# Performance work log

Measured on AMD Instinct MI355X. Metric: run time of the kernel, lower is better.

The kernel has to match this reference:

```python
import jax, jax.numpy as jnp
import numpy as np

T, H, I, E, K = 2048, 1024, 1024, 16, 4
ALPHA, LIMIT, EPS = 1.702, 7.0, 1e-5


def setup_inputs() -> dict:
    key = jax.random.key(0)
    ks = jax.random.split(key, 8)
    s = 0.02  # init scale for weights
    return {
        "x": jax.random.normal(ks[0], (T, H), jnp.float32),
        "norm_scale": jnp.ones((H,), jnp.float32),
        "gate_w": jax.random.normal(ks[1], (E, H), jnp.float32) * s,
        "gate_b": jax.random.normal(ks[2], (E,), jnp.float32) * s,
        "mlp1_w": jax.random.normal(ks[3], (E, 2 * I, H), jnp.float32) * s,
        "mlp1_b": jax.random.normal(ks[4], (E, 2 * I), jnp.float32) * s,
        "mlp2_w": jax.random.normal(ks[5], (E, H, I), jnp.float32) * s,
        "mlp2_b": jax.random.normal(ks[6], (E, H), jnp.float32) * s,
    }


def rmsnorm(x, scale):
    t = x * jax.lax.rsqrt(jnp.mean(x * x, axis=-1, keepdims=True) + EPS)
    return t * scale


def swiglu(h):
    # interleaved gating: even channels -> glu, odd channels -> linear
    glu = jnp.minimum(h[..., ::2], LIMIT)
    lin = jnp.clip(h[..., 1::2], -LIMIT, LIMIT)
    return glu * jax.nn.sigmoid(ALPHA * glu) * (lin + 1.0)


def reference(x, norm_scale, gate_w, gate_b, mlp1_w, mlp1_b, mlp2_w, mlp2_b):
    t = rmsnorm(x, norm_scale)                                   # [T,H]
    g = t @ gate_w.T + gate_b                                    # [T,E]
    vals, idx = jax.lax.top_k(g, K)                              # [T,K]
    w = jax.nn.softmax(vals, axis=-1)                            # [T,K]
    # Dense per-expert FFN (same math as per-token weight gather, computed
    # once per expert then selected -- avoids materializing [T,K,2I,H]).
    h = jnp.einsum('th,ech->tec', t, mlp1_w) + mlp1_b            # [T,E,2I]
    act = swiglu(h)                                              # [T,E,I]
    y = jnp.einsum('tei,ehi->teh', act, mlp2_w) + mlp2_b         # [T,E,H]
    y_sel = jnp.take_along_axis(y, idx[:, :, None], axis=1)      # [T,K,H]
    return x + jnp.einsum('tkh,tk->th', y_sel, w)
```

## Files before the change

### kernel.cpp

```cpp
#include <hip/hip_runtime.h>
#include <hip/hip_bf16.h>
#include <stdint.h>

typedef unsigned short u16;
typedef __attribute__((ext_vector_type(8))) short short8;
typedef __attribute__((ext_vector_type(4))) float f32x4;

#define T_TOK 2048
#define H_DIM 1024
#define E_NUM 16
#define TWO_I 2048
#define I_DIM 1024
#define ALPHA 1.702f
#define LIMIT 7.0f
#define CNT_STRIDE 64

__device__ __forceinline__ u16 f2b(float f) {
    uint32_t x = __builtin_bit_cast(uint32_t, f);
    uint32_t r = x + 0x7fffu + ((x >> 16) & 1u);
    return (u16)(r >> 16);
}
__device__ __forceinline__ short8 pack8(float4 a, float4 b) {
    short8 r;
    r[0] = (short)f2b(a.x); r[1] = (short)f2b(a.y);
    r[2] = (short)f2b(a.z); r[3] = (short)f2b(a.w);
    r[4] = (short)f2b(b.x); r[5] = (short)f2b(b.y);
    r[6] = (short)f2b(b.z); r[7] = (short)f2b(b.w);
    return r;
}

template<typename BT> struct BFrag;
template<> struct BFrag<u16> {
    short8 v;
    __device__ __forceinline__ void load(const u16* p) { v = *(const short8*)p; }
    __device__ __forceinline__ short8 get() const { return v; }
};
template<> struct BFrag<float> {
    float4 a, b;
    __device__ __forceinline__ void load(const float* p) {
        const float4* q = (const float4*)p; a = q[0]; b = q[1];
    }
    __device__ __forceinline__ short8 get() const { return pack8(a, b); }
};

__global__ __launch_bounds__(256) void cvt_kernel(
    const float* __restrict__ in, u16* __restrict__ out, int n4)
{
    int i = blockIdx.x * 256 + threadIdx.x;
    int stride = gridDim.x * 256;
    for (; i < n4; i += stride) {
        float4 v = ((const float4*)in)[i];
        uint32_t lo = (uint32_t)f2b(v.x) | ((uint32_t)f2b(v.y) << 16);
        uint32_t hi = (uint32_t)f2b(v.z) | ((uint32_t)f2b(v.w) << 16);
        uint2 p; p.x = lo; p.y = hi;
        ((uint2*)out)[i] = p;
    }
}

__global__ __launch_bounds__(256) void prep_kernel(
    const float* __restrict__ x, const float* __restrict__ scale,
    const float* __restrict__ gw, const float* __restrict__ gb,
    u16* __restrict__ t_out, int* __restrict__ cnt,
    int* __restrict__ pairs, float* __restrict__ pweight,
    float* __restrict__ out)
{
    const int t = blockIdx.x, tid = threadIdx.x;
    const int lane = tid & 63, wid = tid >> 6;
    __shared__ float red[4];
    __shared__ float g4[4][16];
    __shared__ float gsh[16];
    __shared__ float rstd_sh;

    const float4 xv = ((const float4*)(x + (size_t)t * H_DIM))[tid];
    ((float4*)(out + (size_t)t * H_DIM))[tid] = xv;
    float ss = xv.x*xv.x + xv.y*xv.y + xv.z*xv.z + xv.w*xv.w;
#pragma unroll
    for (int off = 32; off > 0; off >>= 1) ss += __shfl_down(ss, off);
    if (lane == 0) red[wid] = ss;
    __syncthreads();
    if (tid == 0) rstd_sh = rsqrtf((red[0]+red[1]+red[2]+red[3]) * (1.f/1024.f) + 1e-5f);
    __syncthreads();
    const float rstd = rstd_sh;
    const float4 sc = ((const float4*)scale)[tid];
    float4 tv;
    tv.x = xv.x * rstd * sc.x; tv.y = xv.y * rstd * sc.y;
    tv.z = xv.z * rstd * sc.z; tv.w = xv.w * rstd * sc.w;
    {
        uint32_t lo = (uint32_t)f2b(tv.x) | ((uint32_t)f2b(tv.y) << 16);
        uint32_t hi = (uint32_t)f2b(tv.z) | ((uint32_t)f2b(tv.w) << 16);
        uint2 p; p.x = lo; p.y = hi;
        *(uint2*)(t_out + (size_t)t * H_DIM + tid * 4) = p;
    }
    float part[16];
#pragma unroll
    for (int e = 0; e < 16; e++) {
        const float4 w4 = ((const float4*)(gw + (size_t)e * H_DIM))[tid];
        part[e] = tv.x*w4.x + tv.y*w4.y + tv.z*w4.z + tv.w*w4.w;
    }
#pragma unroll
    for (int e = 0; e < 16; e++) {
        float v = part[e];
#pragma unroll
        for (int off = 32; off > 0; off >>= 1) v += __shfl_down(v, off);
        if (lane == 0) g4[wid][e] = v;
    }
    __syncthreads();
    if (tid < 16) gsh[tid] = g4[0][tid] + g4[1][tid] + g4[2][tid] + g4[3][tid] + gb[tid];
    __syncthreads();
    if (tid == 0) {
        unsigned mask = 0;
        float vals[4]; int idxs[4];
#pragma unroll
        for (int k = 0; k < 4; k++) {
            float best = -1e30f; int bi = 0;
            for (int e = 0; e < 16; e++)
                if (!((mask >> e) & 1u) && gsh[e] > best) { best = gsh[e]; bi = e; }
            mask |= 1u << bi; vals[k] = best; idxs[k] = bi;
        }
        float m = vals[0], s = 0.f, w[4];
#pragma unroll
        for (int k = 0; k < 4; k++) { w[k] = __expf(vals[k] - m); s += w[k]; }
        float inv = 1.f / s;
#pragma unroll
        for (int k = 0; k < 4; k++) {
            int slot = atomicAdd(&cnt[idxs[k] * CNT_STRIDE], 1);
            pairs[idxs[k] * 2048 + slot] = t * 4 + k;
            pweight[t * 4 + k] = w[k] * inv;
        }
    }
}

template<typename BT>
__global__ __launch_bounds__(256, 1) void ffn1_kernel(
    const u16* __restrict__ t_ws, const BT* __restrict__ w1,
    const float* __restrict__ b1, const int* __restrict__ cnt,
    const int* __restrict__ pairs, u16* __restrict__ act)
{
    const int e = blockIdx.z, nt = blockIdx.x, mt = blockIdx.y;
    const int cnt_e = cnt[e * CNT_STRIDE];
    if (mt * 128 >= cnt_e) return;
    const int tid = threadIdx.x;

    __shared__ u16 As[128 * 72];
    __shared__ u16 Bs[128 * 72];

    const BT* w1e = w1 + (size_t)e * TWO_I * H_DIM;
    const int* plist = pairs + e * 2048;

    const u16* aptr[4]; const BT* bptr[4]; int soff[4];
#pragma unroll
    for (int i = 0; i < 4; i++) {
        int c = tid + i * 256;
        int r = c >> 3, kc = c & 7;
        int gr = mt * 128 + r;
        int info = (gr < cnt_e) ? plist[gr] : plist[0];
        aptr[i] = t_ws + (size_t)(info >> 2) * H_DIM + kc * 8;
        soff[i] = r * 72 + kc * 8;
        int t16 = r >> 4, l16 = r & 15;
        int hcol = nt * 128 + (t16 >> 1) * 32 + l16 * 2 + (t16 & 1);
        bptr[i] = w1e + (size_t)hcol * H_DIM + kc * 8;
    }

    const int lane = tid & 63, wid = tid >> 6;
    const int wm = wid >> 1, wn = wid & 1;
    const int l15 = lane & 15, quad = lane >> 4;

    f32x4 acc[4][4];
#pragma unroll
    for (int mi = 0; mi < 4; mi++)
#pragma unroll
        for (int ni = 0; ni < 4; ni++) acc[mi][ni] = (f32x4){0.f, 0.f, 0.f, 0.f};

    short8 ga[4]; BFrag<BT> gb[4];
#pragma unroll
    for (int i = 0; i < 4; i++) ga[i] = *(const short8*)(aptr[i]);
#pragma unroll
    for (int i = 0; i < 4; i++) gb[i].load(bptr[i]);

    for (int ki = 0; ki < 16; ki++) {
        __syncthreads();
#pragma unroll
        for (int i = 0; i < 4; i++) *(short8*)(&As[soff[i]]) = ga[i];
#pragma unroll
        for (int i = 0; i < 4; i++) *(short8*)(&Bs[soff[i]]) = gb[i].get();
        __syncthreads();
        if (ki < 15) {
#pragma unroll
            for (int i = 0; i < 4; i++) ga[i] = *(const short8*)(aptr[i] + (ki+1) * 64);
#pragma unroll
            for (int i = 0; i < 4; i++) gb[i].load(bptr[i] + (ki+1) * 64);
        }
#pragma unroll
        for (int ks = 0; ks < 2; ks++) {
            short8 af[4], bfr[4];
#pragma unroll
            for (int mi = 0; mi < 4; mi++)
                af[mi] = *(const short8*)(&As[(wm * 64 + mi * 16 + l15) * 72 + ks * 32 + quad * 8]);
#pragma unroll
            for (int ni = 0; ni < 4; ni++)
                bfr[ni] = *(const short8*)(&Bs[(wn * 64 + ni * 16 + l15) * 72 + ks * 32 + quad * 8]);
#pragma unroll
            for (int mi = 0; mi < 4; mi++)
#pragma unroll
                for (int ni = 0; ni < 4; ni++)
                    acc[mi][ni] = __builtin_amdgcn_mfma_f32_16x16x32_bf16(af[mi], bfr[ni], acc[mi][ni], 0, 0, 0);
        }
    }

#pragma unroll
    for (int mi = 0; mi < 4; mi++) {
        int rloc = wm * 64 + mi * 16 + quad * 4;
        int rinfo[4]; bool rval[4];
#pragma unroll
        for (int rg = 0; rg < 4; rg++) {
            int gr = mt * 128 + rloc + rg;
            rval[rg] = gr < cnt_e;
            rinfo[rg] = rval[rg] ? plist[gr] : 0;
        }
#pragma unroll
        for (int qi = 0; qi < 2; qi++) {
            int actcol = nt * 64 + (wn * 2 + qi) * 16 + l15;
            float be = b1[e * TWO_I + 2 * actcol];
            float bo = b1[e * TWO_I + 2 * actcol + 1];
            f32x4 De = acc[mi][qi * 2], Do = acc[mi][qi * 2 + 1];
#pragma unroll
            for (int rg = 0; rg < 4; rg++) {
                if (!rval[rg]) continue;
                float he = De[rg] + be, ho = Do[rg] + bo;
                float glu = fminf(he, LIMIT);
                float lin = fminf(fmaxf(ho, -LIMIT), LIMIT);
                float a = glu * (1.f / (1.f + __expf(-ALPHA * glu))) * (lin + 1.f);
                act[(size_t)rinfo[rg] * I_DIM + actcol] = f2b(a);
            }
        }
    }
}

template<typename BT>
__global__ __launch_bounds__(256, 1) void ffn2_kernel(
    const u16* __restrict__ act, const BT* __restrict__ w2,
    const float* __restrict__ b2, const int* __restrict__ cnt,
    const int* __restrict__ pairs, const float* __restrict__ pweight,
    float* __restrict__ out)
{
    const int e = blockIdx.z, nt = blockIdx.x, mt = blockIdx.y;
    const int cnt_e = cnt[e * CNT_STRIDE];
    if (mt * 128 >= cnt_e) return;
    const int tid = threadIdx.x;

    __shared__ u16 As[128 * 72];
    __shared__ u16 Bs[128 * 72];

    const BT* w2e = w2 + (size_t)e * H_DIM * I_DIM;
    const int* plist = pairs + e * 2048;

    const u16* aptr[4]; const BT* bptr[4]; int soff[4];
#pragma unroll
    for (int i = 0; i < 4; i++) {
        int c = tid + i * 256;
        int r = c >> 3, kc = c & 7;
        int gr = mt * 128 + r;
        int info = (gr < cnt_e) ? plist[gr] : plist[0];
        aptr[i] = act + (size_t)info * I_DIM + kc * 8;
        soff[i] = r * 72 + kc * 8;
        bptr[i] = w2e + (size_t)(nt * 128 + r) * I_DIM + kc * 8;
    }

    const int lane = tid & 63, wid = tid >> 6;
    const int wm = wid >> 1, wn = wid & 1;
    const int l15 = lane & 15, quad = lane >> 4;

    f32x4 acc[4][4];
#pragma unroll
    for (int mi = 0; mi < 4; mi++)
#pragma unroll
        for (int ni = 0; ni < 4; ni++) acc[mi][ni] = (f32x4){0.f, 0.f, 0.f, 0.f};

    short8 ga[4]; BFrag<BT> gb[4];
#pragma unroll
    for (int i = 0; i < 4; i++) ga[i] = *(const short8*)(aptr[i]);
#pragma unroll
    for (int i = 0; i < 4; i++) gb[i].load(bptr[i]);

    for (int ki = 0; ki < 16; ki++) {
        __syncthreads();
#pragma unroll
        for (int i = 0; i < 4; i++) *(short8*)(&As[soff[i]]) = ga[i];
#pragma unroll
        for (int i = 0; i < 4; i++) *(short8*)(&Bs[soff[i]]) = gb[i].get();
        __syncthreads();
        if (ki < 15) {
#pragma unroll
            for (int i = 0; i < 4; i++) ga[i] = *(const short8*)(aptr[i] + (ki+1) * 64);
#pragma unroll
            for (int i = 0; i < 4; i++) gb[i].load(bptr[i] + (ki+1) * 64);
        }
#pragma unroll
        for (int ks = 0; ks < 2; ks++) {
            short8 af[4], bfr[4];
#pragma unroll
            for (int mi = 0; mi < 4; mi++)
                af[mi] = *(const short8*)(&As[(wm * 64 + mi * 16 + l15) * 72 + ks * 32 + quad * 8]);
#pragma unroll
            for (int ni = 0; ni < 4; ni++)
                bfr[ni] = *(const short8*)(&Bs[(wn * 64 + ni * 16 + l15) * 72 + ks * 32 + quad * 8]);
#pragma unroll
            for (int mi = 0; mi < 4; mi++)
#pragma unroll
                for (int ni = 0; ni < 4; ni++)
                    acc[mi][ni] = __builtin_amdgcn_mfma_f32_16x16x32_bf16(af[mi], bfr[ni], acc[mi][ni], 0, 0, 0);
        }
    }

#pragma unroll
    for (int mi = 0; mi < 4; mi++) {
        int rloc = wm * 64 + mi * 16 + quad * 4;
        int rinfo[4]; bool rval[4]; float wp[4];
#pragma unroll
        for (int rg = 0; rg < 4; rg++) {
            int gr = mt * 128 + rloc + rg;
            rval[rg] = gr < cnt_e;
            rinfo[rg] = rval[rg] ? plist[gr] : 0;
            wp[rg] = rval[rg] ? pweight[rinfo[rg]] : 0.f;
        }
#pragma unroll
        for (int ni = 0; ni < 4; ni++) {
            int hc = nt * 128 + wn * 64 + ni * 16 + l15;
            float bv = b2[e * H_DIM + hc];
#pragma unroll
            for (int rg = 0; rg < 4; rg++) {
                if (!rval[rg]) continue;
                float val = (acc[mi][ni][rg] + bv) * wp[rg];
                atomicAdd(&out[(size_t)(rinfo[rg] >> 2) * H_DIM + hc], val);
            }
        }
    }
}

extern "C" void kernel_launch(void* const* d_in, const int* in_sizes, int n_in,
                              void* d_out, int out_size, void* d_ws, size_t ws_size,
                              hipStream_t stream)
{
    const float* x      = (const float*)d_in[0];
    const float* nscale = (const float*)d_in[1];
    const float* gate_w = (const float*)d_in[2];
    const float* gate_b = (const float*)d_in[3];
    const float* mlp1_w = (const float*)d_in[4];
    const float* mlp1_b = (const float*)d_in[5];
    const float* mlp2_w = (const float*)d_in[6];
    const float* mlp2_b = (const float*)d_in[7];
    float* out = (float*)d_out;

    char* ws = (char*)d_ws;
    u16*   t_ws  = (u16*)(ws);
    u16*   act   = (u16*)(ws + (4ull << 20));
    int*   cnt   = (int*)(ws + (28ull << 20));
    int*   pairs = (int*)(ws + (28ull << 20) + 4096);
    float* pw    = (float*)(ws + (28ull << 20) + 4096 + E_NUM * 2048 * 4);
    u16*   w1b   = (u16*)(ws + (32ull << 20));
    u16*   w2b   = (u16*)(ws + (96ull << 20));

    const bool big = ws_size >= (128ull << 20);

    hipMemsetAsync(cnt, 0, E_NUM * CNT_STRIDE * sizeof(int), stream);

    if (big) {
        cvt_kernel<<<2048, 256, 0, stream>>>(mlp1_w, w1b, E_NUM * TWO_I * H_DIM / 4);
        cvt_kernel<<<2048, 256, 0, stream>>>(mlp2_w, w2b, E_NUM * H_DIM * I_DIM / 4);
    }
    prep_kernel<<<T_TOK, 256, 0, stream>>>(x, nscale, gate_w, gate_b, t_ws, cnt, pairs, pw, out);
    if (big) {
        ffn1_kernel<u16><<<dim3(16, 16, E_NUM), 256, 0, stream>>>(t_ws, w1b, mlp1_b, cnt, pairs, act);
        ffn2_kernel<u16><<<dim3(8, 16, E_NUM), 256, 0, stream>>>(act, w2b, mlp2_b, cnt, pairs, pw, out);
    } else {
        ffn1_kernel<float><<<dim3(16, 16, E_NUM), 256, 0, stream>>>(t_ws, mlp1_w, mlp1_b, cnt, pairs, act);
        ffn2_kernel<float><<<dim3(8, 16, E_NUM), 256, 0, stream>>>(act, mlp2_w, mlp2_b, cnt, pairs, pw, out);
    }
}
```

Baseline: 433.7 us.

## Use direct global-to-LDS loads with XOR swizzle and merge weight conversion kernels

```diff
diff --git a/kernel.cpp b/kernel.cpp
--- a/kernel.cpp
+++ b/kernel.cpp
@@ -27,6 +27,12 @@
     r[4] = (short)f2b(b.x); r[5] = (short)f2b(b.y);
     r[6] = (short)f2b(b.z); r[7] = (short)f2b(b.w);
     return r;
+}
+
+typedef __attribute__((address_space(1))) void gas_void;
+typedef __attribute__((address_space(3))) void las_void;
+__device__ __forceinline__ void gl_lds16(const void* g, void* l) {
+    __builtin_amdgcn_global_load_lds((gas_void*)g, (las_void*)l, 16, 0, 0);
 }
 
 template<typename BT> struct BFrag;
@@ -44,16 +50,21 @@
 };
 
 __global__ __launch_bounds__(256) void cvt_kernel(
-    const float* __restrict__ in, u16* __restrict__ out, int n4)
+    const float* __restrict__ in1, u16* __restrict__ out1, int n1,
+    const float* __restrict__ in2, u16* __restrict__ out2, int n2)
 {
     int i = blockIdx.x * 256 + threadIdx.x;
     int stride = gridDim.x * 256;
-    for (; i < n4; i += stride) {
-        float4 v = ((const float4*)in)[i];
+    int ntot = n1 + n2;
+    for (; i < ntot; i += stride) {
+        const float* in; u16* out; int j;
+        if (i < n1) { in = in1; out = out1; j = i; }
+        else        { in = in2; out = out2; j = i - n1; }
+        float4 v = ((const float4*)in)[j];
         uint32_t lo = (uint32_t)f2b(v.x) | ((uint32_t)f2b(v.y) << 16);
         uint32_t hi = (uint32_t)f2b(v.z) | ((uint32_t)f2b(v.w) << 16);
         uint2 p; p.x = lo; p.y = hi;
-        ((uint2*)out)[i] = p;
+        ((uint2*)out)[j] = p;
     }
 }
 
@@ -141,64 +152,66 @@
     if (mt * 128 >= cnt_e) return;
     const int tid = threadIdx.x;
 
-    __shared__ u16 As[128 * 72];
-    __shared__ u16 Bs[128 * 72];
+    __shared__ u16 As[128 * 64];
+    __shared__ u16 Bs[128 * 64];
 
     const BT* w1e = w1 + (size_t)e * TWO_I * H_DIM;
     const int* plist = pairs + e * 2048;
 
-    const u16* aptr[4]; const BT* bptr[4]; int soff[4];
+    const u16* aptr[4]; const BT* bptr[4]; int ldsoff[4];
 #pragma unroll
     for (int i = 0; i < 4; i++) {
         int c = tid + i * 256;
         int r = c >> 3, kc = c & 7;
+        int kcs = kc ^ (r & 7);
         int gr = mt * 128 + r;
         int info = (gr < cnt_e) ? plist[gr] : plist[0];
-        aptr[i] = t_ws + (size_t)(info >> 2) * H_DIM + kc * 8;
-        soff[i] = r * 72 + kc * 8;
+        aptr[i] = t_ws + (size_t)(info >> 2) * H_DIM + kcs * 8;
+        ldsoff[i] = c * 8;
         int t16 = r >> 4, l16 = r & 15;
         int hcol = nt * 128 + (t16 >> 1) * 32 + l16 * 2 + (t16 & 1);
-        bptr[i] = w1e + (size_t)hcol * H_DIM + kc * 8;
+        bptr[i] = w1e + (size_t)hcol * H_DIM + kcs * 8;
     }
 
     const int lane = tid & 63, wid = tid >> 6;
     const int wm = wid >> 1, wn = wid & 1;
     const int l15 = lane & 15, quad = lane >> 4;
+    const int swz = l15 & 7;
 
     f32x4 acc[4][4];
 #pragma unroll
     for (int mi = 0; mi < 4; mi++)
 #pragma unroll
         for (int ni = 0; ni < 4; ni++) acc[mi][ni] = (f32x4){0.f, 0.f, 0.f, 0.f};
-
-    short8 ga[4]; BFrag<BT> gb[4];
-#pragma unroll
-    for (int i = 0; i < 4; i++) ga[i] = *(const short8*)(aptr[i]);
-#pragma unroll
-    for (int i = 0; i < 4; i++) gb[i].load(bptr[i]);
 
     for (int ki = 0; ki < 16; ki++) {
         __syncthreads();
-#pragma unroll
-        for (int i = 0; i < 4; i++) *(short8*)(&As[soff[i]]) = ga[i];
-#pragma unroll
-        for (int i = 0; i < 4; i++) *(short8*)(&Bs[soff[i]]) = gb[i].get();
+        if constexpr (sizeof(BT) == 2) {
+#pragma unroll
+            for (int i = 0; i < 4; i++) gl_lds16(aptr[i] + ki * 64, &As[ldsoff[i]]);
+#pragma unroll
+            for (int i = 0; i < 4; i++) gl_lds16((const BT*)bptr[i] + ki * 64, &Bs[ldsoff[i]]);
+        } else {
+            short8 ta[4]; BFrag<BT> fb[4];
+#pragma unroll
+            for (int i = 0; i < 4; i++) ta[i] = *(const short8*)(aptr[i] + ki * 64);
+#pragma unroll
+            for (int i = 0; i < 4; i++) fb[i].load(bptr[i] + ki * 64);
+#pragma unroll
+            for (int i = 0; i < 4; i++) *(short8*)(&As[ldsoff[i]]) = ta[i];
+#pragma unroll
+            for (int i = 0; i < 4; i++) *(short8*)(&Bs[ldsoff[i]]) = fb[i].get();
+        }
         __syncthreads();
-        if (ki < 15) {
-#pragma unroll
-            for (int i = 0; i < 4; i++) ga[i] = *(const short8*)(aptr[i] + (ki+1) * 64);
-#pragma unroll
-            for (int i = 0; i < 4; i++) gb[i].load(bptr[i] + (ki+1) * 64);
-        }
 #pragma unroll
         for (int ks = 0; ks < 2; ks++) {
             short8 af[4], bfr[4];
 #pragma unroll
             for (int mi = 0; mi < 4; mi++)
-                af[mi] = *(const short8*)(&As[(wm * 64 + mi * 16 + l15) * 72 + ks * 32 + quad * 8]);
+                af[mi] = *(const short8*)(&As[(wm * 64 + mi * 16 + l15) * 64 + (((ks << 2) + quad) ^ swz) * 8]);
 #pragma unroll
             for (int ni = 0; ni < 4; ni++)
-                bfr[ni] = *(const short8*)(&Bs[(wn * 64 + ni * 16 + l15) * 72 + ks * 32 + quad * 8]);
+                bfr[ni] = *(const short8*)(&Bs[(wn * 64 + ni * 16 + l15) * 64 + (((ks << 2) + quad) ^ swz) * 8]);
 #pragma unroll
             for (int mi = 0; mi < 4; mi++)
 #pragma unroll
@@ -248,62 +261,64 @@
     if (mt * 128 >= cnt_e) return;
     const int tid = threadIdx.x;
 
-    __shared__ u16 As[128 * 72];
-    __shared__ u16 Bs[128 * 72];
+    __shared__ u16 As[128 * 64];
+    __shared__ u16 Bs[128 * 64];
 
     const BT* w2e = w2 + (size_t)e * H_DIM * I_DIM;
     const int* plist = pairs + e * 2048;
 
-    const u16* aptr[4]; const BT* bptr[4]; int soff[4];
+    const u16* aptr[4]; const BT* bptr[4]; int ldsoff[4];
 #pragma unroll
     for (int i = 0; i < 4; i++) {
         int c = tid + i * 256;
         int r = c >> 3, kc = c & 7;
+        int kcs = kc ^ (r & 7);
         int gr = mt * 128 + r;
         int info = (gr < cnt_e) ? plist[gr] : plist[0];
-        aptr[i] = act + (size_t)info * I_DIM + kc * 8;
-        soff[i] = r * 72 + kc * 8;
-        bptr[i] = w2e + (size_t)(nt * 128 + r) * I_DIM + kc * 8;
+        aptr[i] = act + (size_t)info * I_DIM + kcs * 8;
+        ldsoff[i] = c * 8;
+        bptr[i] = w2e + (size_t)(nt * 128 + r) * I_DIM + kcs * 8;
     }
 
     const int lane = tid & 63, wid = tid >> 6;
     const int wm = wid >> 1, wn = wid & 1;
     const int l15 = lane & 15, quad = lane >> 4;
+    const int swz = l15 & 7;
 
     f32x4 acc[4][4];
 #pragma unroll
     for (int mi = 0; mi < 4; mi++)
 #pragma unroll
         for (int ni = 0; ni < 4; ni++) acc[mi][ni] = (f32x4){0.f, 0.f, 0.f, 0.f};
-
-    short8 ga[4]; BFrag<BT> gb[4];
-#pragma unroll
-    for (int i = 0; i < 4; i++) ga[i] = *(const short8*)(aptr[i]);
-#pragma unroll
-    for (int i = 0; i < 4; i++) gb[i].load(bptr[i]);
 
     for (int ki = 0; ki < 16; ki++) {
         __syncthreads();
-#pragma unroll
-        for (int i = 0; i < 4; i++) *(short8*)(&As[soff[i]]) = ga[i];
-#pragma unroll
-        for (int i = 0; i < 4; i++) *(short8*)(&Bs[soff[i]]) = gb[i].get();
+        if constexpr (sizeof(BT) == 2) {
+#pragma unroll
+            for (int i = 0; i < 4; i++) gl_lds16(aptr[i] + ki * 64, &As[ldsoff[i]]);
+#pragma unroll
+            for (int i = 0; i < 4; i++) gl_lds16((const BT*)bptr[i] + ki * 64, &Bs[ldsoff[i]]);
+        } else {
+            short8 ta[4]; BFrag<BT> fb[4];
+#pragma unroll
+            for (int i = 0; i < 4; i++) ta[i] = *(const short8*)(aptr[i] + ki * 64);
+#pragma unroll
+            for (int i = 0; i < 4; i++) fb[i].load(bptr[i] + ki * 64);
+#pragma unroll
+            for (int i = 0; i < 4; i++) *(short8*)(&As[ldsoff[i]]) = ta[i];
+#pragma unroll
+            for (int i = 0; i < 4; i++) *(short8*)(&Bs[ldsoff[i]]) = fb[i].get();
+        }
         __syncthreads();
-        if (ki < 15) {
-#pragma unroll
-            for (int i = 0; i < 4; i++) ga[i] = *(const short8*)(aptr[i] + (ki+1) * 64);
-#pragma unroll
-            for (int i = 0; i < 4; i++) gb[i].load(bptr[i] + (ki+1) * 64);
-        }
 #pragma unroll
         for (int ks = 0; ks < 2; ks++) {
             short8 af[4], bfr[4];
 #pragma unroll
             for (int mi = 0; mi < 4; mi++)
-                af[mi] = *(const short8*)(&As[(wm * 64 + mi * 16 + l15) * 72 + ks * 32 + quad * 8]);
+                af[mi] = *(const short8*)(&As[(wm * 64 + mi * 16 + l15) * 64 + (((ks << 2) + quad) ^ swz) * 8]);
 #pragma unroll
             for (int ni = 0; ni < 4; ni++)
-                bfr[ni] = *(const short8*)(&Bs[(wn * 64 + ni * 16 + l15) * 72 + ks * 32 + quad * 8]);
+                bfr[ni] = *(const short8*)(&Bs[(wn * 64 + ni * 16 + l15) * 64 + (((ks << 2) + quad) ^ swz) * 8]);
 #pragma unroll
             for (int mi = 0; mi < 4; mi++)
 #pragma unroll
@@ -365,8 +380,8 @@
     hipMemsetAsync(cnt, 0, E_NUM * CNT_STRIDE * sizeof(int), stream);
 
     if (big) {
-        cvt_kernel<<<2048, 256, 0, stream>>>(mlp1_w, w1b, E_NUM * TWO_I * H_DIM / 4);
-        cvt_kernel<<<2048, 256, 0, stream>>>(mlp2_w, w2b, E_NUM * H_DIM * I_DIM / 4);
+        cvt_kernel<<<2048, 256, 0, stream>>>(mlp1_w, w1b, E_NUM * TWO_I * H_DIM / 4,
+                                             mlp2_w, w2b, E_NUM * H_DIM * I_DIM / 4);
     }
     prep_kernel<<<T_TOK, 256, 0, stream>>>(x, nscale, gate_w, gate_b, t_ws, cnt, pairs, pw, out);
     if (big) {
```

After: 437.3 us. Within noise of the previous version (+0.8%).
